# Performance work log

Measured on AMD Instinct MI355X. Metric: run time of the kernel, lower is better.

The kernel has to match this reference:

```python
import jax, jax.numpy as jnp
import numpy as np

B, S, DIM = 32, 2048, 384
QK = DIM // 8          # 48
EXP = 2 * DIM          # 768, expand_factor = 2
NUM_BLOCKS = 8         # round(8*log2(1+1.0))
EPS = 1e-5


def setup_inputs() -> dict:
    key = jax.random.key(0)
    k1, k2, k3 = jax.random.split(key, 3)
    x = jax.random.normal(k1, (B, S, DIM), dtype=jnp.float32)
    norm_w = jnp.ones((DIM,), dtype=jnp.float32)  # LayerNorm weight, bias=False
    expand_w = (0.5 / DIM**0.5 / 2.0) * jax.random.normal(k2, (2 * QK + 2 * EXP, DIM), dtype=jnp.float32)
    project_w = (1.0 / DIM**0.5 / 2.0 / NUM_BLOCKS) * jax.random.normal(k3, (DIM, EXP), dtype=jnp.float32)
    pos_mult = jnp.array(1.0, dtype=jnp.float32)
    return {"x": x, "norm_w": norm_w, "expand_w": expand_w, "project_w": project_w, "pos_mult": pos_mult}


def reference(x, norm_w, expand_w, project_w, pos_mult):
    s = x.shape[1]
    residual = x
    # LayerNorm (no bias)
    mu = jnp.mean(x, axis=-1, keepdims=True)
    var = jnp.var(x, axis=-1, keepdims=True)
    xn = (x - mu) * jax.lax.rsqrt(var + EPS) * norm_w
    # fused expand projection -> query, key, linear, pre_gelu
    h = jnp.einsum('bsd,ed->bse', xn, expand_w)  # [B,S,2*QK+2*EXP]
    q = h[..., :QK]
    k = h[..., QK:2 * QK]
    lin = h[..., 2 * QK:2 * QK + EXP]
    pre = h[..., 2 * QK + EXP:]
    geglu = lin * jax.nn.gelu(pre, approximate=False)  # torch F.gelu default = erf
    geglu_local = geglu[..., :EXP - DIM]          # [B,S,EXP-DIM]
    geglu_value = geglu[..., EXP - DIM:]          # [B,S,DIM]
    # ALiBi-like additive causal mask
    idx = jnp.arange(s)
    pbb = (idx[None, :] - idx[:, None]).astype(x.dtype)       # [S,S], j - i (<=0 on allowed past)
    future = idx[None, :] > idx[:, None]                       # triu(diagonal=1)
    attn_mask = jnp.where(future, -jnp.inf, jax.nn.softplus(pos_mult) * pbb)
    # scaled dot product attention (single head, d_qk = QK)
    scores = jnp.einsum('bqd,bkd->bqk', q, k) / jnp.sqrt(jnp.array(QK, dtype=x.dtype))
    probs = jax.nn.softmax(scores + attn_mask[None], axis=-1)
    attention = jnp.einsum('bqk,bkd->bqd', probs, geglu_value)
    out = jnp.einsum('bse,de->bsd', jnp.concatenate([geglu_local, attention], axis=-1), project_w)
    return residual + out
```

## Files before the change

kernel.cpp:

```cpp
#include <hip/hip_runtime.h>
#include <hip/hip_bf16.h>
#include <math.h>

#define S_LEN 2048
#define NBATCH 32
#define DIM 384
#define NTOK (NBATCH * S_LEN)

typedef __hip_bfloat16 bf16;
typedef __attribute__((ext_vector_type(8))) short short8v;
typedef __attribute__((ext_vector_type(4))) float f32x4;
typedef __attribute__((ext_vector_type(2))) unsigned int uint2v;
typedef __attribute__((ext_vector_type(4))) int int4v;
typedef short8v fragT;

#define LDAP 72

__device__ __forceinline__ float bf2f(unsigned short u) {
  union { unsigned int i; float f; } c; c.i = ((unsigned int)u) << 16; return c.f;
}

__global__ __launch_bounds__(256) void conv_kernel(const float* __restrict__ we,
                                                   const float* __restrict__ wp,
                                                   bf16* __restrict__ web,
                                                   bf16* __restrict__ wpb) {
  int i = blockIdx.x * 256 + threadIdx.x;
  int stride = gridDim.x * 256;
  for (int j = i; j < 1632 * 384; j += stride) web[j] = __float2bfloat16(we[j]);
  for (int j = i; j < 384 * 768; j += stride) wpb[j] = __float2bfloat16(wp[j]);
}

__global__ __launch_bounds__(256) void ln_kernel(const float* __restrict__ x,
                                                 const float* __restrict__ nw,
                                                 bf16* __restrict__ xn) {
  int token = blockIdx.x * 4 + (threadIdx.x >> 6);
  int lane = threadIdx.x & 63;
  const float* xr = x + (size_t)token * DIM;
  float v[6];
  float s = 0.f, sq = 0.f;
#pragma unroll
  for (int j = 0; j < 6; ++j) {
    v[j] = xr[lane + j * 64];
    s += v[j];
    sq += v[j] * v[j];
  }
#pragma unroll
  for (int o = 32; o; o >>= 1) {
    s += __shfl_xor(s, o);
    sq += __shfl_xor(sq, o);
  }
  float mu = s * (1.f / DIM);
  float var = sq * (1.f / DIM) - mu * mu;
  float rs = rsqrtf(var + 1e-5f);
  bf16* xo = xn + (size_t)token * DIM;
#pragma unroll
  for (int j = 0; j < 6; ++j) {
    int c = lane + j * 64;
    xo[c] = __float2bfloat16((v[j] - mu) * rs * nw[c]);
  }
}

__global__ __launch_bounds__(256, 2) void expand_wide_kernel(
    const bf16* __restrict__ xn, const bf16* __restrict__ web,
    bf16* __restrict__ qkb, bf16* __restrict__ gl, bf16* __restrict__ gv) {
  __shared__ short As[128 * LDAP];
  __shared__ short Bs[256 * LDAP];
  int t = threadIdx.x;
  int lane = t & 63, w = t >> 6;
  int wr = w >> 1, wc = w & 1;
  int m = lane & 15, g = lane >> 4;

  int bid = blockIdx.x;
  int logical = (bid & 7) * 448 + (bid >> 3);
  int xt = logical / 7, y = logical % 7;
  int row0 = xt * 128;

  auto brow_of = [&](int r) -> int {
    if (y == 0) return (r < 96) ? r : 95;
    int c0 = (y - 1) * 128;
    int half = r >> 7, nn = r & 127;
    return (nn < 64) ? (96 + c0 + half * 64 + nn)
                     : (864 + c0 + half * 64 + (nn - 64));
  };

  auto loadA = [&](int kt, short8v* arg) {
#pragma unroll
    for (int i = 0; i < 4; ++i) {
      int idx = i * 256 + t;
      int r = idx >> 3, c8 = idx & 7;
      arg[i] = *reinterpret_cast<const short8v*>(xn + (size_t)(row0 + r) * 384 + kt * 64 + c8 * 8);
    }
  };
  auto loadB = [&](int kt, short8v* brg) {
#pragma unroll
    for (int i = 0; i < 8; ++i) {
      int idx = i * 256 + t;
      int r = idx >> 3, c8 = idx & 7;
      brg[i] = *reinterpret_cast<const short8v*>(web + (size_t)brow_of(r) * 384 + kt * 64 + c8 * 8);
    }
  };

  f32x4 acc[4][8];
#pragma unroll
  for (int i = 0; i < 4; ++i)
#pragma unroll
    for (int j = 0; j < 8; ++j) acc[i][j] = (f32x4){0.f, 0.f, 0.f, 0.f};

  short8v arg[4], brg[8];
  loadA(0, arg);
  loadB(0, brg);

  for (int kt = 0; kt < 6; ++kt) {
    __syncthreads();
#pragma unroll
    for (int i = 0; i < 4; ++i) {
      int idx = i * 256 + t;
      int r = idx >> 3, c8 = idx & 7;
      *reinterpret_cast<short8v*>(&As[r * LDAP + c8 * 8]) = arg[i];
    }
#pragma unroll
    for (int i = 0; i < 8; ++i) {
      int idx = i * 256 + t;
      int r = idx >> 3, c8 = idx & 7;
      *reinterpret_cast<short8v*>(&Bs[r * LDAP + c8 * 8]) = brg[i];
    }
    __syncthreads();
    if (kt < 5) {
      loadA(kt + 1, arg);
      loadB(kt + 1, brg);
    }
#pragma unroll
    for (int ks = 0; ks < 2; ++ks) {
      int ko = ks * 32 + g * 8;
      fragT af[4], bfv[8];
#pragma unroll
      for (int mi = 0; mi < 4; ++mi)
        af[mi] = *reinterpret_cast<const fragT*>(&As[(wr * 64 + mi * 16 + m) * LDAP + ko]);
#pragma unroll
      for (int ni = 0; ni < 8; ++ni)
        bfv[ni] = *reinterpret_cast<const fragT*>(&Bs[(wc * 128 + ni * 16 + m) * LDAP + ko]);
#pragma unroll
      for (int mi = 0; mi < 4; ++mi)
#pragma unroll
        for (int ni = 0; ni < 8; ++ni)
          acc[mi][ni] = __builtin_amdgcn_mfma_f32_16x16x32_bf16(af[mi], bfv[ni], acc[mi][ni], 0, 0, 0);
    }
  }

  int cl = m, rg = g;
  if (y == 0) {
    if (wc == 0) {
#pragma unroll
      for (int mi = 0; mi < 4; ++mi)
#pragma unroll
        for (int ni = 0; ni < 6; ++ni) {
          int n = ni * 16 + cl;
          if (n < 96) {
#pragma unroll
            for (int r = 0; r < 4; ++r) {
              int token = row0 + wr * 64 + mi * 16 + rg * 4 + r;
              qkb[(size_t)token * 96 + n] = __float2bfloat16(acc[mi][ni][r]);
            }
          }
        }
    }
  } else {
    int c0 = (y - 1) * 128;
#pragma unroll
    for (int mi = 0; mi < 4; ++mi)
#pragma unroll
      for (int ni = 0; ni < 4; ++ni) {
        int c = c0 + wc * 64 + ni * 16 + cl;
#pragma unroll
        for (int r = 0; r < 4; ++r) {
          int token = row0 + wr * 64 + mi * 16 + rg * 4 + r;
          float lin = acc[mi][ni][r];
          float pre = acc[mi][ni + 4][r];
          float z = 0.79788456f * (pre + 0.044715f * pre * pre * pre);
          float gelu = pre * (1.f / (1.f + __expf(-2.f * z)));
          float gval = lin * gelu;
          if (c < 384)
            gl[(size_t)token * DIM + c] = __float2bfloat16(gval);
          else
            gv[(size_t)token * DIM + (c - 384)] = __float2bfloat16(gval);
        }
      }
  }
}

#define ATT_P_OFF 0
#define ATT_Q_OFF 8704
#define ATT_K_OFF 13312
#define ATT_S_OFF 31744
#define ATT_V0_OFF 8704
#define ATT_V1_OFF 36352
#define ATT_SMEM 64000

__global__ __launch_bounds__(256) void attn_mfma_kernel(
    const bf16* __restrict__ qkb, const bf16* __restrict__ gv,
    const float* __restrict__ pos_mult, bf16* __restrict__ ao) {
  __shared__ char smem[ATT_SMEM];
  bf16* P = (bf16*)(smem + ATT_P_OFF);
  bf16* Qs = (bf16*)(smem + ATT_Q_OFF);
  bf16* Ks = (bf16*)(smem + ATT_K_OFF);
  float* Ss = (float*)(smem + ATT_S_OFF);

  int t = threadIdx.x;
  int lane = t & 63;
  int w = t >> 6;
  int batch = blockIdx.x >> 6;
  int q0 = (blockIdx.x & 63) * 32;
  size_t tb = (size_t)batch * S_LEN;
  int jbase = q0 - 96;
  float cmul = log1pf(expf(pos_mult[0]));
  const float rs = 0.14433756729740643f;
  const short8v z8 = (short8v){0, 0, 0, 0, 0, 0, 0, 0};

  {
    int r = t >> 3, c = t & 7;
    short8v v = z8;
    if (c < 6) v = *reinterpret_cast<const short8v*>(qkb + (tb + q0 + r) * 96 + c * 8);
    *reinterpret_cast<short8v*>(Qs + r * LDAP + c * 8) = v;
  }
  {
    int r = t >> 1, h = t & 1;
    int j = jbase + r;
    if (j >= 0) {
      const bf16* krow = qkb + (tb + j) * 96 + 48 + h * 24;
      *reinterpret_cast<short8v*>(Ks + r * LDAP + h * 24) = *reinterpret_cast<const short8v*>(krow);
      *reinterpret_cast<short8v*>(Ks + r * LDAP + h * 24 + 8) = *reinterpret_cast<const short8v*>(krow + 8);
      *reinterpret_cast<short8v*>(Ks + r * LDAP + h * 24 + 16) = *reinterpret_cast<const short8v*>(krow + 16);
    } else {
      *reinterpret_cast<short8v*>(Ks + r * LDAP + h * 24) = z8;
      *reinterpret_cast<short8v*>(Ks + r * LDAP + h * 24 + 8) = z8;
      *reinterpret_cast<short8v*>(Ks + r * LDAP + h * 24 + 16) = z8;
    }
    if (h == 1) {
      *reinterpret_cast<short8v*>(Ks + r * LDAP + 48) = z8;
      *reinterpret_cast<short8v*>(Ks + r * LDAP + 56) = z8;
    }
  }
  __syncthreads();

  int m = lane & 15, g = lane >> 4;

  {
    f32x4 sacc[2][2];
#pragma unroll
    for (int mi = 0; mi < 2; ++mi)
#pragma unroll
      for (int ni = 0; ni < 2; ++ni) sacc[mi][ni] = (f32x4){0.f, 0.f, 0.f, 0.f};
#pragma unroll
    for (int ks = 0; ks < 2; ++ks) {
      int ko = ks * 32 + g * 8;
      fragT aq[2], bk[2];
#pragma unroll
      for (int mi = 0; mi < 2; ++mi)
        aq[mi] = *reinterpret_cast<const fragT*>(Qs + (mi * 16 + m) * LDAP + ko);
#pragma unroll
      for (int ni = 0; ni < 2; ++ni)
        bk[ni] = *reinterpret_cast<const fragT*>(Ks + (w * 32 + ni * 16 + m) * LDAP + ko);
#pragma unroll
      for (int mi = 0; mi < 2; ++mi)
#pragma unroll
        for (int ni = 0; ni < 2; ++ni)
          sacc[mi][ni] = __builtin_amdgcn_mfma_f32_16x16x32_bf16(aq[mi], bk[ni], sacc[mi][ni], 0, 0, 0);
    }
#pragma unroll
    for (int mi = 0; mi < 2; ++mi)
#pragma unroll
      for (int ni = 0; ni < 2; ++ni)
#pragma unroll
        for (int r = 0; r < 4; ++r) {
          int q = mi * 16 + g * 4 + r;
          int key = w * 32 + ni * 16 + m;
          int gi = q0 + q, gj = jbase + key;
          float s = (gj >= 0 && gj <= gi)
                        ? sacc[mi][ni][r] * rs + cmul * (float)(gj - gi)
                        : -INFINITY;
          Ss[q * 132 + key] = s;
        }
  }
  __syncthreads();

  auto stageV = [&](int c, unsigned bufoff) {
    int j = t >> 3;
    int c8 = t & 7;
    int gj = jbase + c * 32 + j;
    bf16* vb = (bf16*)(smem + bufoff);
    const bf16* vrow = gv + (tb + gj) * (size_t)DIM;
#pragma unroll
    for (int it = 0; it < 6; ++it) {
      int dj = c8 + it * 8;
      int d = dj * 8;
      short8v v = z8;
      if (gj >= 0) v = *reinterpret_cast<const short8v*>(vrow + d);
      *reinterpret_cast<short8v*>(vb + ((j >> 2) * 24 + (d >> 4)) * LDAP + (j & 3) * 16 + (d & 15)) = v;
    }
  };

  {
    int sq = t >> 3, sl = t & 7;
    union { float4 f4[4]; float f[16]; } su;
#pragma unroll
    for (int u = 0; u < 4; ++u)
      su.f4[u] = *reinterpret_cast<const float4*>(Ss + sq * 132 + sl * 16 + u * 4);
    __syncthreads();
    float mx = -INFINITY;
#pragma unroll
    for (int e = 0; e < 16; ++e) mx = fmaxf(mx, su.f[e]);
    mx = fmaxf(mx, __shfl_xor(mx, 1));
    mx = fmaxf(mx, __shfl_xor(mx, 2));
    mx = fmaxf(mx, __shfl_xor(mx, 4));
    float pv[16];
    float sum = 0.f;
#pragma unroll
    for (int e = 0; e < 16; ++e) {
      pv[e] = expf(su.f[e] - mx);
      sum += pv[e];
    }
    sum += __shfl_xor(sum, 1);
    sum += __shfl_xor(sum, 2);
    sum += __shfl_xor(sum, 4);
    float inv = 1.f / sum;
    union { bf16 b[16]; short8v s[2]; } pk;
#pragma unroll
    for (int e = 0; e < 16; ++e) pk.b[e] = __float2bfloat16(pv[e] * inv);
    bf16* pr = P + sq * 136 + sl * 16;
    *reinterpret_cast<short8v*>(pr) = pk.s[0];
    *reinterpret_cast<short8v*>(pr + 8) = pk.s[1];
  }
  stageV(0, ATT_V0_OFF);
  __syncthreads();

  f32x4 oacc[2][6];
#pragma unroll
  for (int mi = 0; mi < 2; ++mi)
#pragma unroll
    for (int nt = 0; nt < 6; ++nt) oacc[mi][nt] = (f32x4){0.f, 0.f, 0.f, 0.f};

  unsigned sbase = (unsigned)(size_t)(&smem[0]);
  unsigned lanebase = (unsigned)(((48 * g + 6 * w) * LDAP + m) * 2);

  for (int c = 0; c < 4; ++c) {
    unsigned vaddr = sbase + ((c & 1) ? ATT_V1_OFF : ATT_V0_OFF) + lanebase;
    fragT pa0 = *reinterpret_cast<const fragT*>(P + m * 136 + c * 32 + g * 8);
    fragT pa1 = *reinterpret_cast<const fragT*>(P + (16 + m) * 136 + c * 32 + g * 8);
    uint2v trr[12];
#pragma unroll
    for (int nt = 0; nt < 6; ++nt) {
      asm volatile("ds_read_b64_tr_b16 %0, %1" : "=v"(trr[2 * nt]) : "v"(vaddr + nt * 144));
      asm volatile("ds_read_b64_tr_b16 %0, %1" : "=v"(trr[2 * nt + 1]) : "v"(vaddr + nt * 144 + 3456));
    }
    asm volatile("s_waitcnt lgkmcnt(0)" ::: "memory");
    __builtin_amdgcn_sched_barrier(0);
    if (c < 3) stageV(c + 1, (c & 1) ? ATT_V0_OFF : ATT_V1_OFF);
#pragma unroll
    for (int nt = 0; nt < 6; ++nt) {
      union { int4v i4; fragT f; } u;
      u.i4 = (int4v){(int)trr[2 * nt].x, (int)trr[2 * nt].y,
                     (int)trr[2 * nt + 1].x, (int)trr[2 * nt + 1].y};
      oacc[0][nt] = __builtin_amdgcn_mfma_f32_16x16x32_bf16(pa0, u.f, oacc[0][nt], 0, 0, 0);
      oacc[1][nt] = __builtin_amdgcn_mfma_f32_16x16x32_bf16(pa1, u.f, oacc[1][nt], 0, 0, 0);
    }
    __syncthreads();
  }

#pragma unroll
  for (int mi = 0; mi < 2; ++mi)
#pragma unroll
    for (int nt = 0; nt < 6; ++nt) {
#pragma unroll
      for (int r = 0; r < 4; ++r) {
        int q = mi * 16 + g * 4 + r;
        int d = w * 96 + nt * 16 + m;
        ao[(tb + q0 + q) * (size_t)DIM + d] = __float2bfloat16(oacc[mi][nt][r]);
      }
    }
}

__global__ __launch_bounds__(256) void project_mfma_kernel(
    const bf16* __restrict__ gl, const bf16* __restrict__ at,
    const bf16* __restrict__ wpb, const float* __restrict__ x,
    float* __restrict__ out) {
  __shared__ short As[128 * LDAP];
  __shared__ short Bs[128 * LDAP];
  int t = threadIdx.x;
  int bid = blockIdx.x;
  int logical = (bid & 7) * 192 + (bid >> 3);
  int row0 = (logical / 3) * 128;
  int col0 = (logical % 3) * 128;
  int lane = t & 63;
  int w = t >> 6;
  int wr = w >> 1, wc = w & 1;

  f32x4 acc[4][4];
#pragma unroll
  for (int i = 0; i < 4; ++i)
#pragma unroll
    for (int j = 0; j < 4; ++j) acc[i][j] = (f32x4){0.f, 0.f, 0.f, 0.f};

  int nrow[4];
  int kcol = (t & 7) * 8;
#pragma unroll
  for (int i = 0; i < 4; ++i) nrow[i] = (i * 256 + t) >> 3;

  auto loadA = [&](int kt, short8v* dst) {
    const bf16* ab = (kt < 6) ? gl : at;
    int kk0 = (kt < 6 ? kt : kt - 6) * 64 + kcol;
#pragma unroll
    for (int i = 0; i < 4; ++i)
      dst[i] = *reinterpret_cast<const short8v*>(ab + (size_t)(row0 + nrow[i]) * DIM + kk0);
  };
  auto loadB = [&](int kt, short8v* dst) {
    int kk0 = kt * 64 + kcol;
#pragma unroll
    for (int i = 0; i < 4; ++i)
      dst[i] = *reinterpret_cast<const short8v*>(wpb + (size_t)(col0 + nrow[i]) * 768 + kk0);
  };

  short8v ar[4], br[4];
  loadA(0, ar);
  loadB(0, br);

  for (int kt = 0; kt < 12; ++kt) {
    __syncthreads();
#pragma unroll
    for (int i = 0; i < 4; ++i) {
      *reinterpret_cast<short8v*>(&As[nrow[i] * LDAP + kcol]) = ar[i];
      *reinterpret_cast<short8v*>(&Bs[nrow[i] * LDAP + kcol]) = br[i];
    }
    __syncthreads();
    short8v an[4], bn[4];
    if (kt < 11) {
      loadA(kt + 1, an);
      loadB(kt + 1, bn);
    }
#pragma unroll
    for (int ks = 0; ks < 2; ++ks) {
      fragT af[4], bfv[4];
      int ko = ks * 32 + (lane >> 4) * 8;
#pragma unroll
      for (int mi = 0; mi < 4; ++mi)
        af[mi] = *reinterpret_cast<const fragT*>(&As[(wr * 64 + mi * 16 + (lane & 15)) * LDAP + ko]);
#pragma unroll
      for (int ni = 0; ni < 4; ++ni)
        bfv[ni] = *reinterpret_cast<const fragT*>(&Bs[(wc * 64 + ni * 16 + (lane & 15)) * LDAP + ko]);
#pragma unroll
      for (int mi = 0; mi < 4; ++mi)
#pragma unroll
        for (int ni = 0; ni < 4; ++ni)
          acc[mi][ni] = __builtin_amdgcn_mfma_f32_16x16x32_bf16(af[mi], bfv[ni], acc[mi][ni], 0, 0, 0);
    }
#pragma unroll
    for (int i = 0; i < 4; ++i) { ar[i] = an[i]; br[i] = bn[i]; }
  }

  int cl = lane & 15, rg = lane >> 4;
#pragma unroll
  for (int mi = 0; mi < 4; ++mi)
#pragma unroll
    for (int ni = 0; ni < 4; ++ni) {
      int d = col0 + wc * 64 + ni * 16 + cl;
#pragma unroll
      for (int r = 0; r < 4; ++r) {
        int token = row0 + wr * 64 + mi * 16 + rg * 4 + r;
        out[(size_t)token * DIM + d] = x[(size_t)token * DIM + d] + acc[mi][ni][r];
      }
    }
}

extern "C" void kernel_launch(void* const* d_in, const int* in_sizes, int n_in,
                              void* d_out, int out_size, void* d_ws, size_t ws_size,
                              hipStream_t stream) {
  (void)in_sizes; (void)n_in; (void)out_size; (void)ws_size;
  const float* x = (const float*)d_in[0];
  const float* nw = (const float*)d_in[1];
  const float* we = (const float*)d_in[2];
  const float* wp = (const float*)d_in[3];
  const float* pm = (const float*)d_in[4];
  char* ws = (char*)d_ws;
  bf16* xn = (bf16*)(ws);
  bf16* qk = (bf16*)(ws + 50331648);
  bf16* gl = (bf16*)(ws + 62914560);
  bf16* gv = (bf16*)(ws + 113246208);
  bf16* at = (bf16*)(ws + 163577856);
  bf16* web = (bf16*)(ws + 163577856);
  bf16* wpb = (bf16*)(ws + 213909504);
  float* out = (float*)d_out;

  hipLaunchKernelGGL(conv_kernel, dim3(512), dim3(256), 0, stream, we, wp, web, wpb);
  hipLaunchKernelGGL(ln_kernel, dim3(NTOK / 4), dim3(256), 0, stream, x, nw, xn);
  hipLaunchKernelGGL(expand_wide_kernel, dim3(512 * 7), dim3(256), 0, stream, xn, web, qk, gl, gv);
  hipLaunchKernelGGL(attn_mfma_kernel, dim3(NBATCH * (S_LEN / 32)), dim3(256), 0, stream, qk, gv, pm, at);
  hipLaunchKernelGGL(project_mfma_kernel, dim3(512 * 3), dim3(256), 0, stream, gl, at, wpb, x, out);
}
```

Baseline: 287.6 us.

## Double-buffer LDS in expand and project GEMMs with two-deep register prefetch

Converts the expand and project GEMM kernels to double-buffered shared memory, so there is one barrier per k-step instead of two. Global loads are prefetched two stages ahead into alternating register sets. The expand kernel also shrinks its k-step from 64 to 32 with a narrower LDS pitch, and both kernels raise wave priority around the MFMA blocks. This costs more LDS and registers per block, which could lower occupancy, and the expand kernel now runs twice as many pipeline steps.

```diff
diff --git a/kernel.cpp b/kernel.cpp
--- a/kernel.cpp
+++ b/kernel.cpp
@@ -60,11 +60,12 @@
   }
 }
 
-__global__ __launch_bounds__(256, 2) void expand_wide_kernel(
+#define EBP 40
+__global__ __launch_bounds__(256, 2) void expand_db_kernel(
     const bf16* __restrict__ xn, const bf16* __restrict__ web,
     bf16* __restrict__ qkb, bf16* __restrict__ gl, bf16* __restrict__ gv) {
-  __shared__ short As[128 * LDAP];
-  __shared__ short Bs[256 * LDAP];
+  __shared__ short Abuf[2][128 * EBP];
+  __shared__ short Bbuf[2][256 * EBP];
   int t = threadIdx.x;
   int lane = t & 63, w = t >> 6;
   int wr = w >> 1, wc = w & 1;
@@ -75,29 +76,39 @@
   int xt = logical / 7, y = logical % 7;
   int row0 = xt * 128;
 
-  auto brow_of = [&](int r) -> int {
-    if (y == 0) return (r < 96) ? r : 95;
-    int c0 = (y - 1) * 128;
-    int half = r >> 7, nn = r & 127;
-    return (nn < 64) ? (96 + c0 + half * 64 + nn)
-                     : (864 + c0 + half * 64 + (nn - 64));
-  };
-
-  auto loadA = [&](int kt, short8v* arg) {
-#pragma unroll
-    for (int i = 0; i < 4; ++i) {
-      int idx = i * 256 + t;
-      int r = idx >> 3, c8 = idx & 7;
-      arg[i] = *reinterpret_cast<const short8v*>(xn + (size_t)(row0 + r) * 384 + kt * 64 + c8 * 8);
-    }
-  };
-  auto loadB = [&](int kt, short8v* brg) {
-#pragma unroll
-    for (int i = 0; i < 8; ++i) {
-      int idx = i * 256 + t;
-      int r = idx >> 3, c8 = idx & 7;
-      brg[i] = *reinterpret_cast<const short8v*>(web + (size_t)brow_of(r) * 384 + kt * 64 + c8 * 8);
-    }
+  int aR[2], aS[2], bR[4], bS[4], bRow[4];
+#pragma unroll
+  for (int i = 0; i < 2; ++i) { int idx = i * 256 + t; aR[i] = idx >> 2; aS[i] = idx & 3; }
+#pragma unroll
+  for (int i = 0; i < 4; ++i) {
+    int idx = i * 256 + t;
+    bR[i] = idx >> 2; bS[i] = idx & 3;
+    int r = bR[i], brow;
+    if (y == 0) brow = (r < 96) ? r : 95;
+    else {
+      int c0 = (y - 1) * 128, half = r >> 7, nn = r & 127;
+      brow = (nn < 64) ? (96 + c0 + half * 64 + nn) : (864 + c0 + half * 64 + (nn - 64));
+    }
+    bRow[i] = brow;
+  }
+
+  auto loadA = [&](int kt, short8v* d) {
+#pragma unroll
+    for (int i = 0; i < 2; ++i)
+      d[i] = *reinterpret_cast<const short8v*>(xn + (size_t)(row0 + aR[i]) * 384 + kt * 32 + aS[i] * 8);
+  };
+  auto loadB = [&](int kt, short8v* d) {
+#pragma unroll
+    for (int i = 0; i < 4; ++i)
+      d[i] = *reinterpret_cast<const short8v*>(web + (size_t)bRow[i] * 384 + kt * 32 + bS[i] * 8);
+  };
+  auto writeAB = [&](int p, const short8v* a, const short8v* b) {
+#pragma unroll
+    for (int i = 0; i < 2; ++i)
+      *reinterpret_cast<short8v*>(&Abuf[p][aR[i] * EBP + aS[i] * 8]) = a[i];
+#pragma unroll
+    for (int i = 0; i < 4; ++i)
+      *reinterpret_cast<short8v*>(&Bbuf[p][bR[i] * EBP + bS[i] * 8]) = b[i];
   };
 
   f32x4 acc[4][8];
@@ -106,45 +117,38 @@
 #pragma unroll
     for (int j = 0; j < 8; ++j) acc[i][j] = (f32x4){0.f, 0.f, 0.f, 0.f};
 
-  short8v arg[4], brg[8];
-  loadA(0, arg);
-  loadB(0, brg);
-
-  for (int kt = 0; kt < 6; ++kt) {
+  short8v a0[2], b0[4], a1[2], b1[4];
+  loadA(0, a0); loadB(0, b0);
+  loadA(1, a1); loadB(1, b1);
+  writeAB(0, a0, b0);
+  __syncthreads();
+
+#pragma unroll
+  for (int s = 0; s < 12; ++s) {
+    int p = s & 1;
+    if (s < 11) {
+      if (s & 1) writeAB(p ^ 1, a0, b0);
+      else       writeAB(p ^ 1, a1, b1);
+    }
+    if (s < 10) {
+      if (s & 1) { loadA(s + 2, a1); loadB(s + 2, b1); }
+      else       { loadA(s + 2, a0); loadB(s + 2, b0); }
+    }
+    fragT af[4], bf8[8];
+#pragma unroll
+    for (int mi = 0; mi < 4; ++mi)
+      af[mi] = *reinterpret_cast<const fragT*>(&Abuf[p][(wr * 64 + mi * 16 + m) * EBP + g * 8]);
+#pragma unroll
+    for (int ni = 0; ni < 8; ++ni)
+      bf8[ni] = *reinterpret_cast<const fragT*>(&Bbuf[p][(wc * 128 + ni * 16 + m) * EBP + g * 8]);
+    __builtin_amdgcn_s_setprio(1);
+#pragma unroll
+    for (int mi = 0; mi < 4; ++mi)
+#pragma unroll
+      for (int ni = 0; ni < 8; ++ni)
+        acc[mi][ni] = __builtin_amdgcn_mfma_f32_16x16x32_bf16(af[mi], bf8[ni], acc[mi][ni], 0, 0, 0);
+    __builtin_amdgcn_s_setprio(0);
     __syncthreads();
-#pragma unroll
-    for (int i = 0; i < 4; ++i) {
-      int idx = i * 256 + t;
-      int r = idx >> 3, c8 = idx & 7;
-      *reinterpret_cast<short8v*>(&As[r * LDAP + c8 * 8]) = arg[i];
-    }
-#pragma unroll
-    for (int i = 0; i < 8; ++i) {
-      int idx = i * 256 + t;
-      int r = idx >> 3, c8 = idx & 7;
-      *reinterpret_cast<short8v*>(&Bs[r * LDAP + c8 * 8]) = brg[i];
-    }
-    __syncthreads();
-    if (kt < 5) {
-      loadA(kt + 1, arg);
-      loadB(kt + 1, brg);
-    }
-#pragma unroll
-    for (int ks = 0; ks < 2; ++ks) {
-      int ko = ks * 32 + g * 8;
-      fragT af[4], bfv[8];
-#pragma unroll
-      for (int mi = 0; mi < 4; ++mi)
-        af[mi] = *reinterpret_cast<const fragT*>(&As[(wr * 64 + mi * 16 + m) * LDAP + ko]);
-#pragma unroll
-      for (int ni = 0; ni < 8; ++ni)
-        bfv[ni] = *reinterpret_cast<const fragT*>(&Bs[(wc * 128 + ni * 16 + m) * LDAP + ko]);
-#pragma unroll
-      for (int mi = 0; mi < 4; ++mi)
-#pragma unroll
-        for (int ni = 0; ni < 8; ++ni)
-          acc[mi][ni] = __builtin_amdgcn_mfma_f32_16x16x32_bf16(af[mi], bfv[ni], acc[mi][ni], 0, 0, 0);
-    }
   }
 
   int cl = m, rg = g;
@@ -379,20 +383,46 @@
     }
 }
 
-__global__ __launch_bounds__(256) void project_mfma_kernel(
+__global__ __launch_bounds__(256, 2) void project_db_kernel(
     const bf16* __restrict__ gl, const bf16* __restrict__ at,
     const bf16* __restrict__ wpb, const float* __restrict__ x,
     float* __restrict__ out) {
-  __shared__ short As[128 * LDAP];
-  __shared__ short Bs[128 * LDAP];
+  __shared__ short Abuf[2][128 * LDAP];
+  __shared__ short Bbuf[2][128 * LDAP];
   int t = threadIdx.x;
   int bid = blockIdx.x;
   int logical = (bid & 7) * 192 + (bid >> 3);
   int row0 = (logical / 3) * 128;
   int col0 = (logical % 3) * 128;
-  int lane = t & 63;
-  int w = t >> 6;
+  int lane = t & 63, w = t >> 6;
   int wr = w >> 1, wc = w & 1;
+  int m = lane & 15, g = lane >> 4;
+
+  int rI[4], c8 = t & 7;
+#pragma unroll
+  for (int i = 0; i < 4; ++i) rI[i] = i * 32 + (t >> 3);
+
+  auto loadA = [&](int kt, short8v* d) {
+    const bf16* ab = (kt < 6) ? gl : at;
+    int kk0 = (kt < 6 ? kt : kt - 6) * 64 + c8 * 8;
+#pragma unroll
+    for (int i = 0; i < 4; ++i)
+      d[i] = *reinterpret_cast<const short8v*>(ab + (size_t)(row0 + rI[i]) * DIM + kk0);
+  };
+  auto loadB = [&](int kt, short8v* d) {
+    int kk0 = kt * 64 + c8 * 8;
+#pragma unroll
+    for (int i = 0; i < 4; ++i)
+      d[i] = *reinterpret_cast<const short8v*>(wpb + (size_t)(col0 + rI[i]) * 768 + kk0);
+  };
+  auto writeAB = [&](int p, const short8v* a, const short8v* b) {
+#pragma unroll
+    for (int i = 0; i < 4; ++i)
+      *reinterpret_cast<short8v*>(&Abuf[p][rI[i] * LDAP + c8 * 8]) = a[i];
+#pragma unroll
+    for (int i = 0; i < 4; ++i)
+      *reinterpret_cast<short8v*>(&Bbuf[p][rI[i] * LDAP + c8 * 8]) = b[i];
+  };
 
   f32x4 acc[4][4];
 #pragma unroll
@@ -400,71 +430,52 @@
 #pragma unroll
     for (int j = 0; j < 4; ++j) acc[i][j] = (f32x4){0.f, 0.f, 0.f, 0.f};
 
-  int nrow[4];
-  int kcol = (t & 7) * 8;
-#pragma unroll
-  for (int i = 0; i < 4; ++i) nrow[i] = (i * 256 + t) >> 3;
-
-  auto loadA = [&](int kt, short8v* dst) {
-    const bf16* ab = (kt < 6) ? gl : at;
-    int kk0 = (kt < 6 ? kt : kt - 6) * 64 + kcol;
-#pragma unroll
-    for (int i = 0; i < 4; ++i)
-      dst[i] = *reinterpret_cast<const short8v*>(ab + (size_t)(row0 + nrow[i]) * DIM + kk0);
-  };
-  auto loadB = [&](int kt, short8v* dst) {
-    int kk0 = kt * 64 + kcol;
-#pragma unroll
-    for (int i = 0; i < 4; ++i)
-      dst[i] = *reinterpret_cast<const short8v*>(wpb + (size_t)(col0 + nrow[i]) * 768 + kk0);
-  };
-
-  short8v ar[4], br[4];
-  loadA(0, ar);
-  loadB(0, br);
-
-  for (int kt = 0; kt < 12; ++kt) {
-    __syncthreads();
-#pragma unroll
-    for (int i = 0; i < 4; ++i) {
-      *reinterpret_cast<short8v*>(&As[nrow[i] * LDAP + kcol]) = ar[i];
-      *reinterpret_cast<short8v*>(&Bs[nrow[i] * LDAP + kcol]) = br[i];
-    }
-    __syncthreads();
-    short8v an[4], bn[4];
-    if (kt < 11) {
-      loadA(kt + 1, an);
-      loadB(kt + 1, bn);
+  short8v a0[4], b0[4], a1[4], b1[4];
+  loadA(0, a0); loadB(0, b0);
+  loadA(1, a1); loadB(1, b1);
+  writeAB(0, a0, b0);
+  __syncthreads();
+
+#pragma unroll
+  for (int s = 0; s < 12; ++s) {
+    int p = s & 1;
+    if (s < 11) {
+      if (s & 1) writeAB(p ^ 1, a0, b0);
+      else       writeAB(p ^ 1, a1, b1);
+    }
+    if (s < 10) {
+      if (s & 1) { loadA(s + 2, a1); loadB(s + 2, b1); }
+      else       { loadA(s + 2, a0); loadB(s + 2, b0); }
     }
 #pragma unroll
     for (int ks = 0; ks < 2; ++ks) {
+      int ko = ks * 32 + g * 8;
       fragT af[4], bfv[4];
-      int ko = ks * 32 + (lane >> 4) * 8;
 #pragma unroll
       for (int mi = 0; mi < 4; ++mi)
-        af[mi] = *reinterpret_cast<const fragT*>(&As[(wr * 64 + mi * 16 + (lane & 15)) * LDAP + ko]);
+        af[mi] = *reinterpret_cast<const fragT*>(&Abuf[p][(wr * 64 + mi * 16 + m) * LDAP + ko]);
 #pragma unroll
       for (int ni = 0; ni < 4; ++ni)
-        bfv[ni] = *reinterpret_cast<const fragT*>(&Bs[(wc * 64 + ni * 16 + (lane & 15)) * LDAP + ko]);
+        bfv[ni] = *reinterpret_cast<const fragT*>(&Bbuf[p][(wc * 64 + ni * 16 + m) * LDAP + ko]);
+      __builtin_amdgcn_s_setprio(1);
 #pragma unroll
       for (int mi = 0; mi < 4; ++mi)
 #pragma unroll
         for (int ni = 0; ni < 4; ++ni)
           acc[mi][ni] = __builtin_amdgcn_mfma_f32_16x16x32_bf16(af[mi], bfv[ni], acc[mi][ni], 0, 0, 0);
-    }
-#pragma unroll
-    for (int i = 0; i < 4; ++i) { ar[i] = an[i]; br[i] = bn[i]; }
-  }
-
-  int cl = lane & 15, rg = lane >> 4;
+      __builtin_amdgcn_s_setprio(0);
+    }
+    __syncthreads();
+  }
+
 #pragma unroll
   for (int mi = 0; mi < 4; ++mi)
 #pragma unroll
     for (int ni = 0; ni < 4; ++ni) {
-      int d = col0 + wc * 64 + ni * 16 + cl;
+      int d = col0 + wc * 64 + ni * 16 + m;
 #pragma unroll
       for (int r = 0; r < 4; ++r) {
-        int token = row0 + wr * 64 + mi * 16 + rg * 4 + r;
+        int token = row0 + wr * 64 + mi * 16 + g * 4 + r;
         out[(size_t)token * DIM + d] = x[(size_t)token * DIM + d] + acc[mi][ni][r];
       }
     }
@@ -491,7 +502,7 @@
 
   hipLaunchKernelGGL(conv_kernel, dim3(512), dim3(256), 0, stream, we, wp, web, wpb);
   hipLaunchKernelGGL(ln_kernel, dim3(NTOK / 4), dim3(256), 0, stream, x, nw, xn);
-  hipLaunchKernelGGL(expand_wide_kernel, dim3(512 * 7), dim3(256), 0, stream, xn, web, qk, gl, gv);
+  hipLaunchKernelGGL(expand_db_kernel, dim3(512 * 7), dim3(256), 0, stream, xn, web, qk, gl, gv);
   hipLaunchKernelGGL(attn_mfma_kernel, dim3(NBATCH * (S_LEN / 32)), dim3(256), 0, stream, qk, gv, pm, at);
-  hipLaunchKernelGGL(project_mfma_kernel, dim3(512 * 3), dim3(256), 0, stream, gl, at, wpb, x, out);
-}
+  hipLaunchKernelGGL(project_db_kernel, dim3(512 * 3), dim3(256), 0, stream, gl, at, wpb, x, out);
+}
```

Measured after the change: 279.8 us. 1.03x faster.
